# Performance work log

Measured on AMD Instinct MI355X. Metric: run time of the kernel, lower is better.

Reference implementation:

```python
import jax, jax.numpy as jnp
import numpy as np

MAX_RHO = 12.0
N_THETAS = 16
N_RHOS = 5
G = N_THETAS * N_RHOS          # 80 gaussians
W_NUM = 5                      # weights_num == n_feat -> per-channel conv
OUT_DIM = 80                   # conv_shape = [80, 80]
EPS = 1e-5


def _initial_coords():
    grid_rho = np.linspace(0.0, MAX_RHO, num=N_RHOS + 1)[1:]
    grid_theta = np.linspace(0.0, 2.0 * np.pi, num=N_THETAS + 1)[:-1]
    gr, gt = np.meshgrid(grid_rho, grid_theta, sparse=False)
    return gr.T.flatten().astype(np.float32), gt.T.flatten().astype(np.float32)


def setup_inputs() -> dict:
    key = jax.random.key(0)
    ks = jax.random.split(key, 6)
    B, N, V = 2, 500, 64
    input_feat = jax.random.normal(ks[0], (B, N, V, W_NUM), dtype=jnp.float32)
    rho_coords = jax.random.uniform(ks[1], (B, N, V), dtype=jnp.float32) * MAX_RHO
    theta_coords = jax.random.uniform(ks[2], (B, N, V), dtype=jnp.float32) * (2.0 * np.pi)
    mask = (jax.random.uniform(ks[3], (B, N, V, 1)) > 0.2).astype(jnp.float32)

    mu_r0, mu_t0 = _initial_coords()
    mu_rho = jnp.tile(jnp.asarray(mu_r0)[None, :], (W_NUM, 1))       # [W, G]
    mu_theta = jnp.tile(jnp.asarray(mu_t0)[None, :], (W_NUM, 1))     # [W, G]
    sigma_rho = jnp.full((W_NUM, G), MAX_RHO / 8.0, dtype=jnp.float32)
    sigma_theta = jnp.ones((W_NUM, G), dtype=jnp.float32)

    # VarianceScaling(scale=1, fan_avg, uniform): limit = sqrt(3 / fan_avg)
    limit = np.sqrt(3.0 / ((G + OUT_DIM) / 2.0)).astype(np.float32)
    W_conv = jax.random.uniform(ks[4], (W_NUM, G, OUT_DIM), dtype=jnp.float32,
                                minval=-limit, maxval=limit)
    b_conv = jnp.zeros((W_NUM, OUT_DIM), dtype=jnp.float32)

    return {
        "input_feat": input_feat, "rho_coords": rho_coords,
        "theta_coords": theta_coords, "mask": mask,
        "mu_rho": mu_rho, "mu_theta": mu_theta,
        "sigma_rho": sigma_rho, "sigma_theta": sigma_theta,
        "W_conv": W_conv, "b_conv": b_conv,
        "n_rotations": 16,
    }


def reference(input_feat, rho_coords, theta_coords, mask,
              mu_rho, mu_theta, sigma_rho, sigma_theta,
              W_conv, b_conv, n_rotations):
    # input_feat: [B,N,V,W]; rho/theta: [B,N,V]; mask: [B,N,V,1]
    two_pi = 2.0 * np.pi
    # rho gaussian is rotation-independent -> compute once: [B,N,V,W,G]
    g_rho = jnp.exp(-jnp.square(rho_coords[..., None, None] - mu_rho)
                    / (jnp.square(sigma_rho) + EPS))
    m = mask[..., None]                      # [B,N,V,1,1]

    def one_rotation(k):
        th = jnp.mod(theta_coords + k * (two_pi / n_rotations), two_pi)
        g_th = jnp.exp(-jnp.square(th[..., None, None] - mu_theta)
                       / (jnp.square(sigma_theta) + EPS))    # [B,N,V,W,G]
        gauss = g_rho * g_th * m
        gauss = gauss / (jnp.sum(gauss, axis=2, keepdims=True) + EPS)  # mean over vertices
        # weighted patch aggregation: each weight i sees only feature channel i
        desc = jnp.einsum('bnvwg,bnvw->bnwg', gauss, input_feat)
        return jnp.einsum('bnwg,wgo->bnwo', desc, W_conv) + b_conv     # [B,N,W,O]

    ks = jnp.arange(n_rotations, dtype=jnp.float32)

    def body(carry, k):
        return jnp.maximum(carry, one_rotation(k)), None

    init = one_rotation(ks[0])
    out, _ = jax.lax.scan(body, init, ks[1:])
    return out  # [B, n_samples, weights_num, conv_shape[0]]
```

## Files before the change

### kernel.cpp

```cpp
#include <hip/hip_runtime.h>

#define V 64
#define W 5
#define G 80
#define O 80
#define NROT 16
#define GPAD 104
#define EPSV 1e-5f
#define NLOG2E (-1.4426950408889634f)

#define TSTR 72
#define XSTR 68

using f32x4 = __attribute__((ext_vector_type(4))) float;

__device__ __forceinline__ unsigned short f2bf(float x) {
    unsigned u = __float_as_uint(x);
    unsigned r = (u + 0x7FFFu + ((u >> 16) & 1u)) >> 16;
    return (unsigned short)r;
}
__device__ __forceinline__ float pick5(float a0, float a1, float a2,
                                       float a3, float a4, int r) {
    float x = (r == 1) ? a1 : a0;
    x = (r == 2) ? a2 : x;
    x = (r == 3) ? a3 : x;
    x = (r == 4) ? a4 : x;
    return x;
}

#if __has_builtin(__builtin_amdgcn_mfma_f32_16x16x32_f16)
typedef _Float16 elem_t;
typedef elem_t efrag __attribute__((ext_vector_type(8)));
#define EMFMA(a, b, c) __builtin_amdgcn_mfma_f32_16x16x32_f16((a), (b), (c), 0, 0, 0)
__device__ __forceinline__ unsigned epack(float a, float b) {
    auto r = __builtin_amdgcn_cvt_pkrtz(a, b);
    return __builtin_bit_cast(unsigned, r);
}
__device__ __forceinline__ elem_t ecast(float x) { return (_Float16)x; }
#else
typedef short elem_t;
typedef elem_t efrag __attribute__((ext_vector_type(8)));
#define EMFMA(a, b, c) __builtin_amdgcn_mfma_f32_16x16x32_bf16((a), (b), (c), 0, 0, 0)
__device__ __forceinline__ unsigned epack(float a, float b) {
    return (unsigned)f2bf(a) | ((unsigned)f2bf(b) << 16);
}
__device__ __forceinline__ elem_t ecast(float x) { return (elem_t)f2bf(x); }
#endif

__global__ __launch_bounds__(64) void pack_wc_kernel(
    const float* __restrict__ Wc, unsigned short* __restrict__ wsB)
{
    const int f = blockIdx.x, l = threadIdx.x;
    const int w = f / 15, r = f % 15, ks = r / 5, nt = r % 5;
    const int g0 = ks * 32 + ((l >> 4) << 3);
    const int o  = nt * 16 + (l & 15);
    unsigned v[4];
    #pragma unroll
    for (int i = 0; i < 4; ++i) {
        int ga = g0 + 2 * i, gb = g0 + 2 * i + 1;
        float xa = (ga < G) ? Wc[(w * G + ga) * O + o] : 0.0f;
        float xb = (gb < G) ? Wc[(w * G + gb) * O + o] : 0.0f;
        v[i] = epack(xa, xb);
    }
    *(uint4*)(wsB + ((size_t)f * 64 + l) * 8) = make_uint4(v[0], v[1], v[2], v[3]);
}

__global__ __launch_bounds__(256, 8) void conv_kernel(
    const float* __restrict__ feat,
    const float* __restrict__ rho,
    const float* __restrict__ theta,
    const float* __restrict__ mask,
    const float* __restrict__ mu_rho,
    const float* __restrict__ mu_theta,
    const float* __restrict__ sig_rho,
    const float* __restrict__ sig_theta,
    const unsigned short* __restrict__ wsB,
    const float* __restrict__ bc,
    float* __restrict__ out)
{
    __shared__ __align__(16) float s_x[NROT][XSTR];
    __shared__ __align__(16) float s_fT[W][XSTR];
    __shared__ __align__(16) float s_arg[5][XSTR];
    __shared__ __align__(16) elem_t s_A[32 * TSTR];
    __shared__ __align__(16) elem_t s_descT[W * NROT * GPAD];
    __shared__ float s_ct[16], s_mt[16], s_shift[8], s_sre[8];

    const int tid = threadIdx.x;
    const int p = blockIdx.x;

    const float kstep = 0.39269908169872414f;
    const float two_pi = 6.283185307179586f;
    const float inv_two_pi = 0.15915494309189535f;

    #pragma unroll
    for (int i = tid; i < V * W; i += 256) {
        int v = i / 5, w = i - 5 * (i / 5);
        s_fT[w][v] = feat[p * V * W + i];
    }
    {
        int r = tid >> 6, v = tid & 63;
        float mu_r = mu_rho[r * 16];
        float sr   = sig_rho[r * 16];
        float c_r  = NLOG2E / (sr * sr + EPSV);
        float rv   = rho[p * V + v];
        float mk   = (mask[p * V + v] != 0.0f) ? 0.0f : -1e30f;
        float dr = rv - mu_r;
        float av = fmaf(dr * dr, c_r, mk);
        s_arg[r][v] = av;
        float m = av;
        m = fmaxf(m, __shfl_xor(m, 1));
        m = fmaxf(m, __shfl_xor(m, 2));
        m = fmaxf(m, __shfl_xor(m, 4));
        m = fmaxf(m, __shfl_xor(m, 8));
        m = fmaxf(m, __shfl_xor(m, 16));
        m = fmaxf(m, __shfl_xor(m, 32));
        if (v == 0) {
            float sh = fminf(-m, 60.0f);
            s_shift[r] = sh;
            s_sre[r]   = EPSV * __builtin_amdgcn_exp2f(sh);
        }
    }
    if (tid < 64) {
        int v = tid;
        float mu_r = mu_rho[4 * 16];
        float sr   = sig_rho[4 * 16];
        float c_r  = NLOG2E / (sr * sr + EPSV);
        float rv   = rho[p * V + v];
        float mk   = (mask[p * V + v] != 0.0f) ? 0.0f : -1e30f;
        float dr = rv - mu_r;
        float av = fmaf(dr * dr, c_r, mk);
        s_arg[4][v] = av;
        float m = av;
        m = fmaxf(m, __shfl_xor(m, 1));
        m = fmaxf(m, __shfl_xor(m, 2));
        m = fmaxf(m, __shfl_xor(m, 4));
        m = fmaxf(m, __shfl_xor(m, 8));
        m = fmaxf(m, __shfl_xor(m, 16));
        m = fmaxf(m, __shfl_xor(m, 32));
        if (v == 0) {
            float sh = fminf(-m, 60.0f);
            s_shift[4] = sh;
            s_sre[4]   = EPSV * __builtin_amdgcn_exp2f(sh);
        }
    }
    if (tid < 16) {
        float st = sig_theta[tid];
        s_ct[tid] = NLOG2E / (st * st + EPSV);
        s_mt[tid] = mu_theta[tid];
    }
    #pragma unroll
    for (int i = tid; i < V * NROT; i += 256) {
        int v = i >> 4, k = i & 15;
        float x = theta[p * V + v] + (float)k * kstep;
        x -= floorf(x * inv_two_pi) * two_pi;
        s_x[k][v] = x;
    }
    {
        unsigned* d32 = (unsigned*)s_descT;
        #pragma unroll
        for (int i = tid; i < 80 * 12; i += 256)
            d32[(i / 12) * (GPAD / 2) + 40 + (i % 12)] = 0u;
    }

    int ok = 1;
    #pragma unroll
    for (int i = tid; i < 4 * G; i += 256) {
        int wc2 = 1 + i / 80, g2 = i % 80;
        int gr2 = (g2 >> 4) << 4, gt2 = g2 & 15;
        ok = ok &&
             (mu_rho  [wc2 * G + g2] == mu_rho  [g2]) &&
             (mu_theta[wc2 * G + g2] == mu_theta[g2]) &&
             (sig_rho [wc2 * G + g2] == sig_rho [g2]) &&
             (sig_theta[wc2 * G + g2] == sig_theta[g2]) &&
             (mu_rho  [g2] == mu_rho  [gr2]) &&
             (sig_rho [g2] == sig_rho [gr2]) &&
             (mu_theta[g2] == mu_theta[gt2]) &&
             (sig_theta[g2] == sig_theta[gt2]);
    }
    const int uni = __syncthreads_and(ok);

    const int ww = tid >> 6;
    const int l  = tid & 63;
    const int lg = l >> 4, lc = l & 15;
    const int v0 = lg << 3;

    if (uni) {
        {
            int m = tid >> 3, s = tid & 7;
            unsigned pk0 = 0, pk1 = 0, pk2 = 0, pk3 = 0;
            if (m < 30) {
                int w  = m / 5;
                int rr = (m < 25) ? (m - 5 * w) : (m - 25);
                float sh = s_shift[rr];
                const float* ap = &s_arg[rr][8 * s];
                float4 aa = *(const float4*)ap;
                float4 ab = *(const float4*)(ap + 4);
                float e0 = __builtin_amdgcn_exp2f(aa.x + sh);
                float e1 = __builtin_amdgcn_exp2f(aa.y + sh);
                float e2 = __builtin_amdgcn_exp2f(aa.z + sh);
                float e3 = __builtin_amdgcn_exp2f(aa.w + sh);
                float e4 = __builtin_amdgcn_exp2f(ab.x + sh);
                float e5 = __builtin_amdgcn_exp2f(ab.y + sh);
                float e6 = __builtin_amdgcn_exp2f(ab.z + sh);
                float e7 = __builtin_amdgcn_exp2f(ab.w + sh);
                if (m < 25) {
                    const float* fp = &s_fT[w][8 * s];
                    float4 fa = *(const float4*)fp;
                    float4 fb = *(const float4*)(fp + 4);
                    e0 *= fa.x; e1 *= fa.y; e2 *= fa.z; e3 *= fa.w;
                    e4 *= fb.x; e5 *= fb.y; e6 *= fb.z; e7 *= fb.w;
                }
                pk0 = epack(e0, e1); pk1 = epack(e2, e3);
                pk2 = epack(e4, e5); pk3 = epack(e6, e7);
            }
            *(uint4*)(s_A + m * TSTR + 8 * s) = make_uint4(pk0, pk1, pk2, pk3);
        }
        __syncthreads();

        #pragma unroll 1
        for (int q = 0; q < 4; ++q) {
            const int nt = ww + 4 * q;
            float ct = s_ct[nt], mt = s_mt[nt];
            float bco = -2.0f * ct * mt;
            float cco = ct * mt * mt;
            const float* xr = &s_x[lc][v0];
            float4 xa = *(const float4*)(xr);
            float4 xb = *(const float4*)(xr + 4);
            #define EX(v) __builtin_amdgcn_exp2f(fmaf(fmaf(ct, (v), bco), (v), cco))
            efrag b0 = __builtin_bit_cast(efrag, make_uint4(
                epack(EX(xa.x), EX(xa.y)), epack(EX(xa.z), EX(xa.w)),
                epack(EX(xb.x), EX(xb.y)), epack(EX(xb.z), EX(xb.w))));
            xa = *(const float4*)(xr + 32);
            xb = *(const float4*)(xr + 36);
            efrag b1 = __builtin_bit_cast(efrag, make_uint4(
                epack(EX(xa.x), EX(xa.y)), epack(EX(xa.z), EX(xa.w)),
                epack(EX(xb.x), EX(xb.y)), epack(EX(xb.z), EX(xb.w))));
            #undef EX

            efrag a00 = *(const efrag*)(s_A + lc * TSTR + (lg << 3));
            efrag a01 = *(const efrag*)(s_A + lc * TSTR + 32 + (lg << 3));
            efrag a10 = *(const efrag*)(s_A + (16 + lc) * TSTR + (lg << 3));
            efrag a11 = *(const efrag*)(s_A + (16 + lc) * TSTR + 32 + (lg << 3));

            f32x4 z = {0.f, 0.f, 0.f, 0.f};
            f32x4 c0 = EMFMA(a00, b0, z);
            c0 = EMFMA(a01, b1, c0);
            f32x4 c1 = EMFMA(a10, b0, z);
            c1 = EMFMA(a11, b1, c1);

            float dn0 = __shfl(c1[1], 32 + lc);
            float dn1 = __shfl(c1[2], 32 + lc);
            float dn2 = __shfl(c1[3], 32 + lc);
            float dn3 = __shfl(c1[0], 48 + lc);
            float dn4 = __shfl(c1[1], 48 + lc);
            float i0 = __builtin_amdgcn_rcpf(dn0 + s_sre[0]);
            float i1 = __builtin_amdgcn_rcpf(dn1 + s_sre[1]);
            float i2 = __builtin_amdgcn_rcpf(dn2 + s_sre[2]);
            float i3 = __builtin_amdgcn_rcpf(dn3 + s_sre[3]);
            float i4 = __builtin_amdgcn_rcpf(dn4 + s_sre[4]);

            #pragma unroll
            for (int i = 0; i < 4; ++i) {
                int m = lg * 4 + i;
                int w0 = m / 5, r0 = m - 5 * (m / 5);
                float inv = pick5(i0, i1, i2, i3, i4, r0);
                s_descT[(w0 * 16 + lc) * GPAD + r0 * 16 + nt] = ecast(c0[i] * inv);
            }
            #pragma unroll
            for (int i = 0; i < 4; ++i) {
                int m2 = 16 + lg * 4 + i;
                if (m2 < 25) {
                    int w1 = m2 / 5, r1 = m2 - 5 * (m2 / 5);
                    float inv = pick5(i0, i1, i2, i3, i4, r1);
                    s_descT[(w1 * 16 + lc) * GPAD + r1 * 16 + nt] = ecast(c1[i] * inv);
                }
            }
        }
    } else {
        #pragma unroll 1
        for (int i = tid; i < 320; i += 256) {
            int g = i % 80, j = i / 80;
            #pragma unroll 1
            for (int w = 0; w < W; ++w) {
                const float mu_r = mu_rho[w * G + g];
                const float sr   = sig_rho[w * G + g];
                const float c_sr = NLOG2E / (sr * sr + EPSV);
                const float mu_t = mu_theta[w * G + g];
                const float st   = sig_theta[w * G + g];
                const float c_st = NLOG2E / (st * st + EPSV);
                float den[4] = {0.f, 0.f, 0.f, 0.f};
                float nm[4]  = {0.f, 0.f, 0.f, 0.f};
                for (int v = 0; v < V; ++v) {
                    float rv  = rho[p * V + v];
                    float mk  = (mask[p * V + v] != 0.0f) ? 0.0f : -1e30f;
                    float fw  = s_fT[w][v];
                    float dr = rv - mu_r;
                    float argr = fmaf(dr * dr, c_sr, mk);
                    #pragma unroll
                    for (int kk = 0; kk < 4; ++kk) {
                        float x = s_x[4 * j + kk][v];
                        float t = x - mu_t;
                        float e = __builtin_amdgcn_exp2f(fmaf(t * t, c_st, argr));
                        den[kk] += e;
                        nm[kk] = fmaf(e, fw, nm[kk]);
                    }
                }
                #pragma unroll
                for (int kk = 0; kk < 4; ++kk)
                    s_descT[(w * 16 + 4 * j + kk) * GPAD + g] =
                        ecast(nm[kk] * __builtin_amdgcn_rcpf(den[kk] + EPSV));
            }
        }
    }

    __syncthreads();

    #pragma unroll 1
    for (int u = ww; u < 25; u += 4) {
        int w = u / 5, nt = u % 5;
        efrag a0 = *(const efrag*)(s_descT + (w * 16 + lc) * GPAD + (lg << 3));
        efrag a1 = *(const efrag*)(s_descT + (w * 16 + lc) * GPAD + 32 + (lg << 3));
        efrag a2 = *(const efrag*)(s_descT + (w * 16 + lc) * GPAD + 64 + (lg << 3));
        const unsigned short* bp =
            wsB + ((size_t)(((w * 3 + 0) * 5 + nt) * 64 + l)) * 8;
        efrag b0 = *(const efrag*)bp;
        efrag b1 = *(const efrag*)(bp + 5 * 64 * 8);
        efrag b2 = *(const efrag*)(bp + 10 * 64 * 8);
        f32x4 acc = {0.f, 0.f, 0.f, 0.f};
        acc = EMFMA(a0, b0, acc);
        acc = EMFMA(a1, b1, acc);
        acc = EMFMA(a2, b2, acc);
        float m1 = fmaxf(fmaxf(acc[0], acc[1]), fmaxf(acc[2], acc[3]));
        m1 = fmaxf(m1, __shfl_xor(m1, 16));
        m1 = fmaxf(m1, __shfl_xor(m1, 32));
        if (l < 16) {
            int oo = nt * 16 + l;
            out[p * (W * O) + w * O + oo] = m1 + bc[w * O + oo];
        }
    }
}

extern "C" void kernel_launch(void* const* d_in, const int* in_sizes, int n_in,
                              void* d_out, int out_size, void* d_ws, size_t ws_size,
                              hipStream_t stream) {
    const float* feat      = (const float*)d_in[0];
    const float* rho       = (const float*)d_in[1];
    const float* theta     = (const float*)d_in[2];
    const float* mask      = (const float*)d_in[3];
    const float* mu_rho    = (const float*)d_in[4];
    const float* mu_theta  = (const float*)d_in[5];
    const float* sig_rho   = (const float*)d_in[6];
    const float* sig_theta = (const float*)d_in[7];
    const float* Wc        = (const float*)d_in[8];
    const float* bc        = (const float*)d_in[9];
    float* outp            = (float*)d_out;

    const int np = in_sizes[1] / V;
    unsigned short* ws = (unsigned short*)d_ws;

    pack_wc_kernel<<<75, 64, 0, stream>>>(Wc, ws);
    conv_kernel<<<np, 256, 0, stream>>>(feat, rho, theta, mask, mu_rho, mu_theta,
                                        sig_rho, sig_theta, ws, bc, outp);
}
```

Before: 26.45 us.

## Use bf16 for second GEMM, hoist A fragments, unroll rotation loop, add setprio

Descriptors and conv weights are now stored as bf16 and the second GEMM uses the bf16 MFMA explicitly, while the first GEMM keeps the f16 path. A-fragment LDS loads, s_sre values and the index arithmetic are hoisted out of the rotation-tile loop, and that loop is fully unrolled. The theta exponent is now computed as ct*(x-mt)^2 instead of the expanded quadratic, and s_setprio brackets are added around the MFMA groups. Launch bounds drop the occupancy hint from 8 to 4, which gives more register headroom but lowers the guaranteed occupancy. The software f2bf rounding costs more ALU work than the cvt_pkrtz f16 path it replaces.

```diff
diff --git a/kernel.cpp b/kernel.cpp
--- a/kernel.cpp
+++ b/kernel.cpp
@@ -12,7 +12,8 @@
 #define TSTR 72
 #define XSTR 68
 
-using f32x4 = __attribute__((ext_vector_type(4))) float;
+using bf16x8 = __attribute__((ext_vector_type(8))) short;
+using f32x4  = __attribute__((ext_vector_type(4))) float;
 
 __device__ __forceinline__ unsigned short f2bf(float x) {
     unsigned u = __float_as_uint(x);
@@ -36,7 +37,6 @@
     auto r = __builtin_amdgcn_cvt_pkrtz(a, b);
     return __builtin_bit_cast(unsigned, r);
 }
-__device__ __forceinline__ elem_t ecast(float x) { return (_Float16)x; }
 #else
 typedef short elem_t;
 typedef elem_t efrag __attribute__((ext_vector_type(8)));
@@ -44,7 +44,6 @@
 __device__ __forceinline__ unsigned epack(float a, float b) {
     return (unsigned)f2bf(a) | ((unsigned)f2bf(b) << 16);
 }
-__device__ __forceinline__ elem_t ecast(float x) { return (elem_t)f2bf(x); }
 #endif
 
 __global__ __launch_bounds__(64) void pack_wc_kernel(
@@ -54,18 +53,16 @@
     const int w = f / 15, r = f % 15, ks = r / 5, nt = r % 5;
     const int g0 = ks * 32 + ((l >> 4) << 3);
     const int o  = nt * 16 + (l & 15);
-    unsigned v[4];
+    unsigned short v[8];
     #pragma unroll
-    for (int i = 0; i < 4; ++i) {
-        int ga = g0 + 2 * i, gb = g0 + 2 * i + 1;
-        float xa = (ga < G) ? Wc[(w * G + ga) * O + o] : 0.0f;
-        float xb = (gb < G) ? Wc[(w * G + gb) * O + o] : 0.0f;
-        v[i] = epack(xa, xb);
-    }
-    *(uint4*)(wsB + ((size_t)f * 64 + l) * 8) = make_uint4(v[0], v[1], v[2], v[3]);
-}
-
-__global__ __launch_bounds__(256, 8) void conv_kernel(
+    for (int i = 0; i < 8; ++i) {
+        int g = g0 + i;
+        v[i] = (g < G) ? f2bf(Wc[(w * G + g) * O + o]) : (unsigned short)0;
+    }
+    *(uint4*)(wsB + ((size_t)f * 64 + l) * 8) = *(const uint4*)v;
+}
+
+__global__ __launch_bounds__(256, 4) void conv_kernel(
     const float* __restrict__ feat,
     const float* __restrict__ rho,
     const float* __restrict__ theta,
@@ -81,8 +78,8 @@
     __shared__ __align__(16) float s_x[NROT][XSTR];
     __shared__ __align__(16) float s_fT[W][XSTR];
     __shared__ __align__(16) float s_arg[5][XSTR];
-    __shared__ __align__(16) elem_t s_A[32 * TSTR];
-    __shared__ __align__(16) elem_t s_descT[W * NROT * GPAD];
+    __shared__ __align__(16) unsigned short s_A[32 * TSTR];
+    __shared__ __align__(16) unsigned short s_descT[W * NROT * GPAD];
     __shared__ float s_ct[16], s_mt[16], s_shift[8], s_sre[8];
 
     const int tid = threadIdx.x;
@@ -182,7 +179,6 @@
     const int ww = tid >> 6;
     const int l  = tid & 63;
     const int lg = l >> 4, lc = l & 15;
-    const int v0 = lg << 3;
 
     if (uni) {
         {
@@ -213,66 +209,85 @@
                 pk0 = epack(e0, e1); pk1 = epack(e2, e3);
                 pk2 = epack(e4, e5); pk3 = epack(e6, e7);
             }
-            *(uint4*)(s_A + m * TSTR + 8 * s) = make_uint4(pk0, pk1, pk2, pk3);
+            *(uint4*)((elem_t*)s_A + m * TSTR + 8 * s) =
+                make_uint4(pk0, pk1, pk2, pk3);
         }
         __syncthreads();
 
-        #pragma unroll 1
+        const elem_t* EA = (const elem_t*)s_A;
+        efrag a00 = *(const efrag*)(EA + lc * TSTR + (lg << 3));
+        efrag a01 = *(const efrag*)(EA + lc * TSTR + 32 + (lg << 3));
+        efrag a10 = *(const efrag*)(EA + (16 + lc) * TSTR + (lg << 3));
+        efrag a11 = *(const efrag*)(EA + (16 + lc) * TSTR + 32 + (lg << 3));
+        const float sre0 = s_sre[0], sre1 = s_sre[1], sre2 = s_sre[2],
+                    sre3 = s_sre[3], sre4 = s_sre[4];
+
+        int w0[4], r0[4], w1[4], r1[4];
+        bool ok1[4];
+        #pragma unroll
+        for (int i = 0; i < 4; ++i) {
+            int m = lg * 4 + i;
+            w0[i] = m / 5; r0[i] = m - 5 * w0[i];
+            int m2 = 16 + lg * 4 + i;
+            ok1[i] = (m2 < 25);
+            int mm = ok1[i] ? m2 : 24;
+            w1[i] = mm / 5; r1[i] = mm - 5 * w1[i];
+        }
+
+        #pragma unroll
         for (int q = 0; q < 4; ++q) {
             const int nt = ww + 4 * q;
             float ct = s_ct[nt], mt = s_mt[nt];
-            float bco = -2.0f * ct * mt;
-            float cco = ct * mt * mt;
-            const float* xr = &s_x[lc][v0];
+            const float* xr = &s_x[lc][lg << 3];
             float4 xa = *(const float4*)(xr);
             float4 xb = *(const float4*)(xr + 4);
-            #define EX(v) __builtin_amdgcn_exp2f(fmaf(fmaf(ct, (v), bco), (v), cco))
-            efrag b0 = __builtin_bit_cast(efrag, make_uint4(
-                epack(EX(xa.x), EX(xa.y)), epack(EX(xa.z), EX(xa.w)),
-                epack(EX(xb.x), EX(xb.y)), epack(EX(xb.z), EX(xb.w))));
-            xa = *(const float4*)(xr + 32);
-            xb = *(const float4*)(xr + 36);
-            efrag b1 = __builtin_bit_cast(efrag, make_uint4(
-                epack(EX(xa.x), EX(xa.y)), epack(EX(xa.z), EX(xa.w)),
-                epack(EX(xb.x), EX(xb.y)), epack(EX(xb.z), EX(xb.w))));
+            float4 xc = *(const float4*)(xr + 32);
+            float4 xd = *(const float4*)(xr + 36);
+            float d;
+            #define EX(v) (d = (v) - mt, __builtin_amdgcn_exp2f(ct * d * d))
+            unsigned u0 = epack(EX(xa.x), EX(xa.y));
+            unsigned u1 = epack(EX(xa.z), EX(xa.w));
+            unsigned u2 = epack(EX(xb.x), EX(xb.y));
+            unsigned u3 = epack(EX(xb.z), EX(xb.w));
+            efrag b0 = __builtin_bit_cast(efrag, make_uint4(u0, u1, u2, u3));
+            u0 = epack(EX(xc.x), EX(xc.y));
+            u1 = epack(EX(xc.z), EX(xc.w));
+            u2 = epack(EX(xd.x), EX(xd.y));
+            u3 = epack(EX(xd.z), EX(xd.w));
+            efrag b1 = __builtin_bit_cast(efrag, make_uint4(u0, u1, u2, u3));
             #undef EX
 
-            efrag a00 = *(const efrag*)(s_A + lc * TSTR + (lg << 3));
-            efrag a01 = *(const efrag*)(s_A + lc * TSTR + 32 + (lg << 3));
-            efrag a10 = *(const efrag*)(s_A + (16 + lc) * TSTR + (lg << 3));
-            efrag a11 = *(const efrag*)(s_A + (16 + lc) * TSTR + 32 + (lg << 3));
-
             f32x4 z = {0.f, 0.f, 0.f, 0.f};
+            __builtin_amdgcn_s_setprio(1);
             f32x4 c0 = EMFMA(a00, b0, z);
             c0 = EMFMA(a01, b1, c0);
             f32x4 c1 = EMFMA(a10, b0, z);
             c1 = EMFMA(a11, b1, c1);
+            __builtin_amdgcn_s_setprio(0);
 
             float dn0 = __shfl(c1[1], 32 + lc);
             float dn1 = __shfl(c1[2], 32 + lc);
             float dn2 = __shfl(c1[3], 32 + lc);
             float dn3 = __shfl(c1[0], 48 + lc);
             float dn4 = __shfl(c1[1], 48 + lc);
-            float i0 = __builtin_amdgcn_rcpf(dn0 + s_sre[0]);
-            float i1 = __builtin_amdgcn_rcpf(dn1 + s_sre[1]);
-            float i2 = __builtin_amdgcn_rcpf(dn2 + s_sre[2]);
-            float i3 = __builtin_amdgcn_rcpf(dn3 + s_sre[3]);
-            float i4 = __builtin_amdgcn_rcpf(dn4 + s_sre[4]);
+            float i0 = __builtin_amdgcn_rcpf(dn0 + sre0);
+            float i1 = __builtin_amdgcn_rcpf(dn1 + sre1);
+            float i2 = __builtin_amdgcn_rcpf(dn2 + sre2);
+            float i3 = __builtin_amdgcn_rcpf(dn3 + sre3);
+            float i4 = __builtin_amdgcn_rcpf(dn4 + sre4);
 
             #pragma unroll
             for (int i = 0; i < 4; ++i) {
-                int m = lg * 4 + i;
-                int w0 = m / 5, r0 = m - 5 * (m / 5);
-                float inv = pick5(i0, i1, i2, i3, i4, r0);
-                s_descT[(w0 * 16 + lc) * GPAD + r0 * 16 + nt] = ecast(c0[i] * inv);
+                float inv = pick5(i0, i1, i2, i3, i4, r0[i]);
+                s_descT[(w0[i] * 16 + lc) * GPAD + r0[i] * 16 + nt] =
+                    f2bf(c0[i] * inv);
             }
             #pragma unroll
             for (int i = 0; i < 4; ++i) {
-                int m2 = 16 + lg * 4 + i;
-                if (m2 < 25) {
-                    int w1 = m2 / 5, r1 = m2 - 5 * (m2 / 5);
-                    float inv = pick5(i0, i1, i2, i3, i4, r1);
-                    s_descT[(w1 * 16 + lc) * GPAD + r1 * 16 + nt] = ecast(c1[i] * inv);
+                if (ok1[i]) {
+                    float inv = pick5(i0, i1, i2, i3, i4, r1[i]);
+                    s_descT[(w1[i] * 16 + lc) * GPAD + r1[i] * 16 + nt] =
+                        f2bf(c1[i] * inv);
                 }
             }
         }
@@ -308,7 +323,7 @@
                 #pragma unroll
                 for (int kk = 0; kk < 4; ++kk)
                     s_descT[(w * 16 + 4 * j + kk) * GPAD + g] =
-                        ecast(nm[kk] * __builtin_amdgcn_rcpf(den[kk] + EPSV));
+                        f2bf(nm[kk] * __builtin_amdgcn_rcpf(den[kk] + EPSV));
             }
         }
     }
@@ -318,18 +333,26 @@
     #pragma unroll 1
     for (int u = ww; u < 25; u += 4) {
         int w = u / 5, nt = u % 5;
-        efrag a0 = *(const efrag*)(s_descT + (w * 16 + lc) * GPAD + (lg << 3));
-        efrag a1 = *(const efrag*)(s_descT + (w * 16 + lc) * GPAD + 32 + (lg << 3));
-        efrag a2 = *(const efrag*)(s_descT + (w * 16 + lc) * GPAD + 64 + (lg << 3));
+        efrag af0 = *(const efrag*)((const elem_t*)s_descT +
+                                    (w * 16 + lc) * GPAD + (lg << 3));
+        efrag af1 = *(const efrag*)((const elem_t*)s_descT +
+                                    (w * 16 + lc) * GPAD + 32 + (lg << 3));
+        efrag af2 = *(const efrag*)((const elem_t*)s_descT +
+                                    (w * 16 + lc) * GPAD + 64 + (lg << 3));
         const unsigned short* bp =
             wsB + ((size_t)(((w * 3 + 0) * 5 + nt) * 64 + l)) * 8;
-        efrag b0 = *(const efrag*)bp;
-        efrag b1 = *(const efrag*)(bp + 5 * 64 * 8);
-        efrag b2 = *(const efrag*)(bp + 10 * 64 * 8);
+        bf16x8 b0 = *(const bf16x8*)bp;
+        bf16x8 b1 = *(const bf16x8*)(bp + 5 * 64 * 8);
+        bf16x8 b2 = *(const bf16x8*)(bp + 10 * 64 * 8);
         f32x4 acc = {0.f, 0.f, 0.f, 0.f};
-        acc = EMFMA(a0, b0, acc);
-        acc = EMFMA(a1, b1, acc);
-        acc = EMFMA(a2, b2, acc);
+        __builtin_amdgcn_s_setprio(1);
+        acc = __builtin_amdgcn_mfma_f32_16x16x32_bf16(
+                  __builtin_bit_cast(bf16x8, af0), b0, acc, 0, 0, 0);
+        acc = __builtin_amdgcn_mfma_f32_16x16x32_bf16(
+                  __builtin_bit_cast(bf16x8, af1), b1, acc, 0, 0, 0);
+        acc = __builtin_amdgcn_mfma_f32_16x16x32_bf16(
+                  __builtin_bit_cast(bf16x8, af2), b2, acc, 0, 0, 0);
+        __builtin_amdgcn_s_setprio(0);
         float m1 = fmaxf(fmaxf(acc[0], acc[1]), fmaxf(acc[2], acc[3]));
         m1 = fmaxf(m1, __shfl_xor(m1, 16));
         m1 = fmaxf(m1, __shfl_xor(m1, 32));
```

After: 24.19 us. 1.09x faster.
